# Kernel tuning notes

Measured on AMD Instinct MI355X. Metric: run time of the kernel, lower is better.

## Reference

```python
import jax, jax.numpy as jnp
import numpy as np

B, A, V, D = 16, 1024, 1024, 512


def setup_inputs() -> dict:
    key = jax.random.key(0)
    k1, k2 = jax.random.split(key)
    audio_encoded = jax.random.normal(k1, (B, A, D), dtype=jnp.float32)
    visual_encoded = jax.random.normal(k2, (B, V, D), dtype=jnp.float32)
    return {"audio_encoded": audio_encoded, "visual_encoded": visual_encoded}


def reference(audio_encoded, visual_encoded):
    # Batched pairwise L2 distance: out[b, a, v] = ||audio[b,a] - visual[b,v]||_2
    # Fused ||a||^2 + ||v||^2 - 2 a.v formulation (single batched GEMM) replacing
    # the original per-(batch, audio-frame) Python loop of diff/pow/sum/sqrt.
    a_sq = jnp.sum(audio_encoded * audio_encoded, axis=-1)   # [B, A]
    v_sq = jnp.sum(visual_encoded * visual_encoded, axis=-1)  # [B, V]
    cross = jnp.einsum("bad,bvd->bav", audio_encoded, visual_encoded)  # [B, A, V]
    dist_sq = a_sq[:, :, None] + v_sq[:, None, :] - 2.0 * cross
    dist_sq = jnp.maximum(dist_sq, 0.0)  # clamp fp round-off negatives
    l2_features = jnp.sqrt(dist_sq)  # [B, A, V]
    return l2_features
```

## Files before the change

### kernel.cpp

```cpp
#include <hip/hip_runtime.h>
#include <hip/hip_bf16.h>
#include <stdint.h>

typedef __attribute__((ext_vector_type(8))) short short8;
typedef __attribute__((ext_vector_type(4))) float fv4;
typedef __attribute__((ext_vector_type(4))) int   iv4;

constexpr int B_ = 16, A_ = 1024, V_ = 1024, D_ = 512;
constexpr int ROWS_A = B_ * A_;
constexpr int ROWS_T = 2 * ROWS_A;
constexpr size_t BF_BYTES_ONE = (size_t)ROWS_A * D_ * 2;
constexpr size_t WS_NEED = 2 * BF_BYTES_ONE + (size_t)ROWS_T * 4;

__device__ __forceinline__ unsigned f2bf(float f) {
    unsigned u = __builtin_bit_cast(unsigned, f);
    return (u + 0x7fffu + ((u >> 16) & 1u)) >> 16;
}

__global__ void __launch_bounds__(256)
convert_kernel(const float* __restrict__ audio, const float* __restrict__ visual,
               ushort* __restrict__ abf, ushort* __restrict__ vbf,
               float* __restrict__ normA, float* __restrict__ normV)
{
    const int lane = threadIdx.x & 63;
    const int wv   = (blockIdx.x * 256 + threadIdx.x) >> 6;
    const int nw   = (gridDim.x * 256) >> 6;

    for (int row = wv; row < ROWS_T; row += nw) {
        const float* src; ushort* dst; float* nd; int r;
        if (row < ROWS_A) { src = audio;  dst = abf; nd = normA; r = row; }
        else              { src = visual; dst = vbf; nd = normV; r = row - ROWS_A; }

        const float* p = src + (size_t)r * D_ + lane * 8;
        fv4 x0 = *(const fv4*)p;
        fv4 x1 = *(const fv4*)(p + 4);

        float s = 0.f;
#pragma unroll
        for (int i = 0; i < 4; ++i) s += x0[i] * x0[i] + x1[i] * x1[i];

        iv4 w;
        w[0] = (int)(f2bf(x0[0]) | (f2bf(x0[1]) << 16));
        w[1] = (int)(f2bf(x0[2]) | (f2bf(x0[3]) << 16));
        w[2] = (int)(f2bf(x1[0]) | (f2bf(x1[1]) << 16));
        w[3] = (int)(f2bf(x1[2]) | (f2bf(x1[3]) << 16));
        *(iv4*)(dst + (size_t)r * D_ + lane * 8) = w;

#pragma unroll
        for (int m = 1; m < 64; m <<= 1) s += __shfl_xor(s, m, 64);
        if (lane == 0) nd[r] = s;
    }
}

__device__ __forceinline__ void gload16(const void* g, void* l) {
    __builtin_amdgcn_global_load_lds((const __attribute__((address_space(1))) void*)g,
                                     (__attribute__((address_space(3))) void*)l,
                                     16, 0, 0);
}

__global__ void __launch_bounds__(256, 4)
gemm_kernel(const ushort* __restrict__ abf, const ushort* __restrict__ vbf,
            const float* __restrict__ normA, const float* __restrict__ normV,
            float* __restrict__ out)
{
    __shared__ __align__(16) char sA[128 * 128];
    __shared__ __align__(16) char sV[128 * 128];
    __shared__ float lnrm[256];

    const int t    = threadIdx.x;
    const int lane = t & 63;
    const int w    = t >> 6;
    const int wm   = w >> 1;
    const int wn   = w & 1;

    const int orig = blockIdx.x;
    const int wg   = (orig & 7) * 128 + (orig >> 3);
    const int b    = wg >> 6;
    const int tt   = wg & 63;
    const int ab   = tt >> 3;
    const int vb   = tt & 7;

    const ushort* Ag = abf + ((size_t)b * A_ + (size_t)ab * 128) * D_;
    const ushort* Vg = vbf + ((size_t)b * V_ + (size_t)vb * 128) * D_;

    const int rl = lane >> 3;
    const int cs = (lane & 7) ^ rl;

    fv4 acc[4][4];
#pragma unroll
    for (int i = 0; i < 4; ++i)
#pragma unroll
        for (int j = 0; j < 4; ++j) acc[i][j] = fv4{0.f, 0.f, 0.f, 0.f};

    const int frow = lane & 15;
    const int fg   = lane >> 4;
    const int xk   = frow & 7;

    for (int kt = 0; kt < D_ / 64; ++kt) {
#pragma unroll
        for (int i = 0; i < 4; ++i) {
            const int row = i * 32 + w * 8 + rl;
            gload16(Ag + (size_t)row * D_ + kt * 64 + cs * 8, sA + (i * 32 + w * 8) * 128);
            gload16(Vg + (size_t)row * D_ + kt * 64 + cs * 8, sV + (i * 32 + w * 8) * 128);
        }
        __syncthreads();

#pragma unroll
        for (int kk = 0; kk < 2; ++kk) {
            short8 af[4], vf[4];
#pragma unroll
            for (int m = 0; m < 4; ++m) {
                const int r = wm * 64 + m * 16 + frow;
                af[m] = *(const short8*)(sA + r * 128 + (((kk * 4 + fg) ^ xk) << 4));
            }
#pragma unroll
            for (int n = 0; n < 4; ++n) {
                const int r = wn * 64 + n * 16 + frow;
                vf[n] = *(const short8*)(sV + r * 128 + (((kk * 4 + fg) ^ xk) << 4));
            }
#pragma unroll
            for (int m = 0; m < 4; ++m)
#pragma unroll
                for (int n = 0; n < 4; ++n)
                    acc[m][n] = __builtin_amdgcn_mfma_f32_16x16x32_bf16(
                        af[m], vf[n], acc[m][n], 0, 0, 0);
        }
        __syncthreads();
    }

    if (t < 128) lnrm[t]       = normA[(size_t)b * A_ + ab * 128 + t];
    else         lnrm[t]       = normV[(size_t)b * V_ + vb * 128 + (t - 128)];
    __syncthreads();

    float* Ob = out + (size_t)b * A_ * V_ + ((size_t)ab * 128) * V_ + vb * 128;
#pragma unroll
    for (int m = 0; m < 4; ++m) {
#pragma unroll
        for (int n = 0; n < 4; ++n) {
            const int col = wn * 64 + n * 16 + frow;
            const float vsq = lnrm[128 + col];
#pragma unroll
            for (int j = 0; j < 4; ++j) {
                const int row = wm * 64 + m * 16 + fg * 4 + j;
                float d2 = lnrm[row] + vsq - 2.f * acc[m][n][j];
                Ob[(size_t)row * V_ + col] = sqrtf(fmaxf(d2, 0.f));
            }
        }
    }
}

__device__ __forceinline__ iv4 pack8(fv4 x, fv4 y) {
    iv4 r;
    r[0] = (int)(f2bf(x[0]) | (f2bf(x[1]) << 16));
    r[1] = (int)(f2bf(x[2]) | (f2bf(x[3]) << 16));
    r[2] = (int)(f2bf(y[0]) | (f2bf(y[1]) << 16));
    r[3] = (int)(f2bf(y[2]) | (f2bf(y[3]) << 16));
    return r;
}
__device__ __forceinline__ int slot_addr(int r, int g) {
    return r * 64 + (((g) ^ ((r >> 1) & 3)) << 4);
}

__global__ void __launch_bounds__(256)
l2dist_fused(const float* __restrict__ audio, const float* __restrict__ visual,
             float* __restrict__ out)
{
    __shared__ __align__(16) char sA[128 * 64];
    __shared__ __align__(16) char sV[128 * 64];
    __shared__ float pA[128][4];
    __shared__ float pV[128][4];
    __shared__ float nA[128];
    __shared__ float nV[128];

    const int t = threadIdx.x, lane = t & 63, wave = t >> 6;
    const int wm = wave >> 1, wn = wave & 1;
    const int vb = blockIdx.x, ab = blockIdx.y, b = blockIdx.z;
    const int r0 = t >> 2, g = t & 3;

    const float* Ap = audio  + ((size_t)b * A_ + (size_t)ab * 128) * D_;
    const float* Vp = visual + ((size_t)b * V_ + (size_t)vb * 128) * D_;

    fv4 acc[4][4];
#pragma unroll
    for (int i = 0; i < 4; ++i)
#pragma unroll
        for (int j = 0; j < 4; ++j) acc[i][j] = fv4{0.f, 0.f, 0.f, 0.f};
    float psA0 = 0.f, psA1 = 0.f, psV0 = 0.f, psV1 = 0.f;
    const int frow = lane & 15, fg = lane >> 4;

    for (int kt = 0; kt < 16; ++kt) {
        const int koff = kt * 32 + g * 8;
        fv4 a0 = *(const fv4*)(Ap + (size_t)r0 * D_ + koff);
        fv4 a1 = *(const fv4*)(Ap + (size_t)r0 * D_ + koff + 4);
        fv4 a2 = *(const fv4*)(Ap + (size_t)(r0 + 64) * D_ + koff);
        fv4 a3 = *(const fv4*)(Ap + (size_t)(r0 + 64) * D_ + koff + 4);
        fv4 v0 = *(const fv4*)(Vp + (size_t)r0 * D_ + koff);
        fv4 v1 = *(const fv4*)(Vp + (size_t)r0 * D_ + koff + 4);
        fv4 v2 = *(const fv4*)(Vp + (size_t)(r0 + 64) * D_ + koff);
        fv4 v3 = *(const fv4*)(Vp + (size_t)(r0 + 64) * D_ + koff + 4);
#pragma unroll
        for (int i = 0; i < 4; ++i) {
            psA0 += a0[i] * a0[i] + a1[i] * a1[i];
            psA1 += a2[i] * a2[i] + a3[i] * a3[i];
            psV0 += v0[i] * v0[i] + v1[i] * v1[i];
            psV1 += v2[i] * v2[i] + v3[i] * v3[i];
        }
        iv4 wa0 = pack8(a0, a1), wa1 = pack8(a2, a3);
        iv4 wv0 = pack8(v0, v1), wv1 = pack8(v2, v3);
        __syncthreads();
        *(iv4*)(sA + slot_addr(r0, g)) = wa0;
        *(iv4*)(sA + slot_addr(r0 + 64, g)) = wa1;
        *(iv4*)(sV + slot_addr(r0, g)) = wv0;
        *(iv4*)(sV + slot_addr(r0 + 64, g)) = wv1;
        __syncthreads();
        short8 af[4], bfr[4];
#pragma unroll
        for (int m = 0; m < 4; ++m)
            af[m] = *(const short8*)(sA + slot_addr(wm * 64 + m * 16 + frow, fg));
#pragma unroll
        for (int n = 0; n < 4; ++n)
            bfr[n] = *(const short8*)(sV + slot_addr(wn * 64 + n * 16 + frow, fg));
#pragma unroll
        for (int m = 0; m < 4; ++m)
#pragma unroll
            for (int n = 0; n < 4; ++n)
                acc[m][n] = __builtin_amdgcn_mfma_f32_16x16x32_bf16(af[m], bfr[n], acc[m][n], 0, 0, 0);
    }

    pA[r0][g] = psA0; pA[r0 + 64][g] = psA1;
    pV[r0][g] = psV0; pV[r0 + 64][g] = psV1;
    __syncthreads();
    if (t < 128) nA[t] = pA[t][0] + pA[t][1] + pA[t][2] + pA[t][3];
    else { int r = t - 128; nV[r] = pV[r][0] + pV[r][1] + pV[r][2] + pV[r][3]; }
    __syncthreads();

    float* Ob = out + (size_t)b * A_ * V_ + ((size_t)ab * 128) * V_ + vb * 128;
#pragma unroll
    for (int m = 0; m < 4; ++m)
#pragma unroll
        for (int n = 0; n < 4; ++n) {
            const int col = wn * 64 + n * 16 + frow;
            const float vsq = nV[col];
#pragma unroll
            for (int j = 0; j < 4; ++j) {
                const int row = wm * 64 + m * 16 + fg * 4 + j;
                float d2 = nA[row] + vsq - 2.f * acc[m][n][j];
                Ob[(size_t)row * V_ + col] = sqrtf(fmaxf(d2, 0.f));
            }
        }
}

extern "C" void kernel_launch(void* const* d_in, const int* in_sizes, int n_in,
                              void* d_out, int out_size, void* d_ws, size_t ws_size,
                              hipStream_t stream) {
    const float* audio  = (const float*)d_in[0];
    const float* visual = (const float*)d_in[1];
    float* out = (float*)d_out;

    if (ws_size >= WS_NEED) {
        char* ws = (char*)d_ws;
        ushort* abf = (ushort*)ws;
        ushort* vbf = (ushort*)(ws + BF_BYTES_ONE);
        float*  nA  = (float*)(ws + 2 * BF_BYTES_ONE);
        float*  nV  = nA + ROWS_A;
        convert_kernel<<<2048, 256, 0, stream>>>(audio, visual, abf, vbf, nA, nV);
        gemm_kernel<<<1024, 256, 0, stream>>>(abf, vbf, nA, nV, out);
    } else {
        dim3 grid(8, 8, 16);
        l2dist_fused<<<grid, 256, 0, stream>>>(audio, visual, out);
    }
}
```

Baseline: 46.33 us.

## Replace 128x128 GEMM with double-buffered 256x256 tile kernel using 512 threads

Swaps the 128x128 bf16 MFMA GEMM for a 256x256-tile kernel with 8 waves. It double-buffers LDS so the next K-slice's global-to-LDS loads overlap the current compute, uses inline ds_read_b128 with staged fragment loads and s_setprio around MFMA bursts, and preloads the norms before the main loop. The aim is more data reuse per tile and hidden load latency. The cost is 128KB of LDS per block and only 256 workgroups, which is about one per CU, so occupancy and tail balance may suffer.

Result: slower. 49.54 us (+6.9%).

```diff
diff --git a/kernel.cpp b/kernel.cpp
--- a/kernel.cpp
+++ b/kernel.cpp
@@ -9,8 +9,8 @@
 constexpr int B_ = 16, A_ = 1024, V_ = 1024, D_ = 512;
 constexpr int ROWS_A = B_ * A_;
 constexpr int ROWS_T = 2 * ROWS_A;
-constexpr size_t BF_BYTES_ONE = (size_t)ROWS_A * D_ * 2;
-constexpr size_t WS_NEED = 2 * BF_BYTES_ONE + (size_t)ROWS_T * 4;
+constexpr size_t BF_ONE = (size_t)ROWS_A * D_ * 2;
+constexpr size_t WS_NEED = 2 * BF_ONE + (size_t)ROWS_T * 4;
 
 __device__ __forceinline__ unsigned f2bf(float f) {
     unsigned u = __builtin_bit_cast(unsigned, f);
@@ -57,91 +57,164 @@
                                      (__attribute__((address_space(3))) void*)l,
                                      16, 0, 0);
 }
-
-__global__ void __launch_bounds__(256, 4)
-gemm_kernel(const ushort* __restrict__ abf, const ushort* __restrict__ vbf,
-            const float* __restrict__ normA, const float* __restrict__ normV,
-            float* __restrict__ out)
+__device__ __forceinline__ unsigned lds_addr(const void* p) {
+    return (unsigned)(unsigned long long)(__attribute__((address_space(3))) const char*)p;
+}
+__device__ __forceinline__ short8 dsr128(unsigned a) {
+    short8 r;
+    asm volatile("ds_read_b128 %0, %1" : "=v"(r) : "v"(a));
+    return r;
+}
+#define LGK0() asm volatile("s_waitcnt lgkmcnt(0)")
+#define VMC0() asm volatile("s_waitcnt vmcnt(0)")
+#define SB0()  __builtin_amdgcn_sched_barrier(0)
+#define BAR()  __builtin_amdgcn_s_barrier()
+
+__global__ void __launch_bounds__(512, 2)
+gemm256(const ushort* __restrict__ abf, const ushort* __restrict__ vbf,
+        const float* __restrict__ normA, const float* __restrict__ normV,
+        float* __restrict__ out)
 {
-    __shared__ __align__(16) char sA[128 * 128];
-    __shared__ __align__(16) char sV[128 * 128];
-    __shared__ float lnrm[256];
-
-    const int t    = threadIdx.x;
-    const int lane = t & 63;
-    const int w    = t >> 6;
-    const int wm   = w >> 1;
-    const int wn   = w & 1;
+    __shared__ __align__(16) char sA[2][256 * 128];
+    __shared__ __align__(16) char sB[2][256 * 128];
+    __shared__ float lnrm[512];
+
+    const int t = threadIdx.x, lane = t & 63, w = t >> 6;
+    const int wm = w >> 2, wn = w & 3;
 
     const int orig = blockIdx.x;
-    const int wg   = (orig & 7) * 128 + (orig >> 3);
-    const int b    = wg >> 6;
-    const int tt   = wg & 63;
-    const int ab   = tt >> 3;
-    const int vb   = tt & 7;
-
-    const ushort* Ag = abf + ((size_t)b * A_ + (size_t)ab * 128) * D_;
-    const ushort* Vg = vbf + ((size_t)b * V_ + (size_t)vb * 128) * D_;
+    const int wg   = (orig & 7) * 32 + (orig >> 3);
+    const int b = wg >> 4, tile = wg & 15, ab = tile >> 2, vb = tile & 3;
+
+    const ushort* Ag = abf + ((size_t)b * A_ + ab * 256) * D_;
+    const ushort* Vg = vbf + ((size_t)b * V_ + vb * 256) * D_;
 
     const int rl = lane >> 3;
     const int cs = (lane & 7) ^ rl;
-
-    fv4 acc[4][4];
-#pragma unroll
-    for (int i = 0; i < 4; ++i)
-#pragma unroll
-        for (int j = 0; j < 4; ++j) acc[i][j] = fv4{0.f, 0.f, 0.f, 0.f};
-
-    const int frow = lane & 15;
-    const int fg   = lane >> 4;
-    const int xk   = frow & 7;
-
-    for (int kt = 0; kt < D_ / 64; ++kt) {
-#pragma unroll
-        for (int i = 0; i < 4; ++i) {
-            const int row = i * 32 + w * 8 + rl;
-            gload16(Ag + (size_t)row * D_ + kt * 64 + cs * 8, sA + (i * 32 + w * 8) * 128);
-            gload16(Vg + (size_t)row * D_ + kt * 64 + cs * 8, sV + (i * 32 + w * 8) * 128);
-        }
-        __syncthreads();
-
-#pragma unroll
-        for (int kk = 0; kk < 2; ++kk) {
-            short8 af[4], vf[4];
-#pragma unroll
-            for (int m = 0; m < 4; ++m) {
-                const int r = wm * 64 + m * 16 + frow;
-                af[m] = *(const short8*)(sA + r * 128 + (((kk * 4 + fg) ^ xk) << 4));
+    const ushort* asrc = Ag + (size_t)(w * 8 + rl) * D_ + cs * 8;
+    const ushort* vsrc = Vg + (size_t)(w * 8 + rl) * D_ + cs * 8;
+
+    if (t < 256) lnrm[t] = normA[(size_t)b * A_ + ab * 256 + t];
+    else         lnrm[t] = normV[(size_t)b * V_ + vb * 256 + (t - 256)];
+    __syncthreads();
+
+    fv4 acc[8][4];
+#pragma unroll
+    for (int m = 0; m < 8; ++m)
+#pragma unroll
+        for (int n = 0; n < 4; ++n) acc[m][n] = fv4{0.f, 0.f, 0.f, 0.f};
+
+    const int frow = lane & 15, fg = lane >> 4, xk = frow & 7;
+    const unsigned sAbase = lds_addr(&sA[0][0]);
+    const unsigned sBbase = lds_addr(&sB[0][0]);
+    const unsigned arow = (unsigned)((wm * 128 + frow) * 128);
+    const unsigned brow = (unsigned)((wn * 64 + frow) * 128);
+    const unsigned c0 = (unsigned)(((0 + fg) ^ xk) << 4);
+    const unsigned c1 = (unsigned)(((4 + fg) ^ xk) << 4);
+
+#pragma unroll
+    for (int h = 0; h < 4; ++h) {
+        gload16(asrc + (size_t)h * 64 * D_, (char*)sA[0] + (h * 64 + w * 8) * 128);
+        gload16(vsrc + (size_t)h * 64 * D_, (char*)sB[0] + (h * 64 + w * 8) * 128);
+    }
+    VMC0();
+
+    short8 av[4][2], bv[4][2];
+
+    for (int kt = 0; kt < 8; ++kt) {
+        BAR();
+        const int cur = kt & 1;
+
+        if (kt < 7) {
+            const size_t soff = (size_t)(kt + 1) * 64;
+            char* da = (char*)sA[cur ^ 1] + w * 8 * 128;
+            char* db = (char*)sB[cur ^ 1] + w * 8 * 128;
+#pragma unroll
+            for (int h = 0; h < 4; ++h) {
+                gload16(asrc + (size_t)h * 64 * D_ + soff, da + h * 64 * 128);
+                gload16(vsrc + (size_t)h * 64 * D_ + soff, db + h * 64 * 128);
             }
-#pragma unroll
-            for (int n = 0; n < 4; ++n) {
-                const int r = wn * 64 + n * 16 + frow;
-                vf[n] = *(const short8*)(sV + r * 128 + (((kk * 4 + fg) ^ xk) << 4));
-            }
+        }
+
+        const unsigned Ab = sAbase + (unsigned)cur * 32768u + arow;
+        const unsigned Bb = sBbase + (unsigned)cur * 32768u + brow;
+
+#pragma unroll
+        for (int m = 0; m < 4; ++m) {
+            av[m][0] = dsr128(Ab + m * 2048 + c0);
+            av[m][1] = dsr128(Ab + m * 2048 + c1);
+        }
+#pragma unroll
+        for (int n = 0; n < 2; ++n) {
+            bv[n][0] = dsr128(Bb + n * 2048 + c0);
+            bv[n][1] = dsr128(Bb + n * 2048 + c1);
+        }
+        LGK0(); SB0();
+        __builtin_amdgcn_s_setprio(1);
+#pragma unroll
+        for (int k = 0; k < 2; ++k)
 #pragma unroll
             for (int m = 0; m < 4; ++m)
 #pragma unroll
-                for (int n = 0; n < 4; ++n)
-                    acc[m][n] = __builtin_amdgcn_mfma_f32_16x16x32_bf16(
-                        af[m], vf[n], acc[m][n], 0, 0, 0);
-        }
-        __syncthreads();
-    }
-
-    if (t < 128) lnrm[t]       = normA[(size_t)b * A_ + ab * 128 + t];
-    else         lnrm[t]       = normV[(size_t)b * V_ + vb * 128 + (t - 128)];
-    __syncthreads();
-
-    float* Ob = out + (size_t)b * A_ * V_ + ((size_t)ab * 128) * V_ + vb * 128;
-#pragma unroll
-    for (int m = 0; m < 4; ++m) {
+                for (int n = 0; n < 2; ++n)
+                    acc[m][n] = __builtin_amdgcn_mfma_f32_16x16x32_bf16(av[m][k], bv[n][k], acc[m][n], 0, 0, 0);
+        __builtin_amdgcn_s_setprio(0);
+
+#pragma unroll
+        for (int n = 2; n < 4; ++n) {
+            bv[n][0] = dsr128(Bb + n * 2048 + c0);
+            bv[n][1] = dsr128(Bb + n * 2048 + c1);
+        }
+        LGK0(); SB0();
+        __builtin_amdgcn_s_setprio(1);
+#pragma unroll
+        for (int k = 0; k < 2; ++k)
+#pragma unroll
+            for (int m = 0; m < 4; ++m)
+#pragma unroll
+                for (int n = 2; n < 4; ++n)
+                    acc[m][n] = __builtin_amdgcn_mfma_f32_16x16x32_bf16(av[m][k], bv[n][k], acc[m][n], 0, 0, 0);
+        __builtin_amdgcn_s_setprio(0);
+
+#pragma unroll
+        for (int m = 0; m < 4; ++m) {
+            av[m][0] = dsr128(Ab + (m + 4) * 2048 + c0);
+            av[m][1] = dsr128(Ab + (m + 4) * 2048 + c1);
+        }
+        LGK0(); SB0();
+        __builtin_amdgcn_s_setprio(1);
+#pragma unroll
+        for (int k = 0; k < 2; ++k)
+#pragma unroll
+            for (int m = 0; m < 4; ++m)
+#pragma unroll
+                for (int n = 2; n < 4; ++n)
+                    acc[m + 4][n] = __builtin_amdgcn_mfma_f32_16x16x32_bf16(av[m][k], bv[n][k], acc[m + 4][n], 0, 0, 0);
+        __builtin_amdgcn_s_setprio(0);
+
+        __builtin_amdgcn_s_setprio(1);
+#pragma unroll
+        for (int k = 0; k < 2; ++k)
+#pragma unroll
+            for (int m = 0; m < 4; ++m)
+#pragma unroll
+                for (int n = 0; n < 2; ++n)
+                    acc[m + 4][n] = __builtin_amdgcn_mfma_f32_16x16x32_bf16(av[m][k], bv[n][k], acc[m + 4][n], 0, 0, 0);
+        __builtin_amdgcn_s_setprio(0);
+
+        VMC0();
+    }
+
+    float* Ob = out + (size_t)b * A_ * V_ + (size_t)(ab * 256) * V_ + vb * 256;
+#pragma unroll
+    for (int m = 0; m < 8; ++m) {
 #pragma unroll
         for (int n = 0; n < 4; ++n) {
             const int col = wn * 64 + n * 16 + frow;
-            const float vsq = lnrm[128 + col];
+            const float vsq = lnrm[256 + col];
 #pragma unroll
             for (int j = 0; j < 4; ++j) {
-                const int row = wm * 64 + m * 16 + fg * 4 + j;
+                const int row = wm * 128 + m * 16 + fg * 4 + j;
                 float d2 = lnrm[row] + vsq - 2.f * acc[m][n][j];
                 Ob[(size_t)row * V_ + col] = sqrtf(fmaxf(d2, 0.f));
             }
@@ -165,8 +238,8 @@
 l2dist_fused(const float* __restrict__ audio, const float* __restrict__ visual,
              float* __restrict__ out)
 {
-    __shared__ __align__(16) char sA[128 * 64];
-    __shared__ __align__(16) char sV[128 * 64];
+    __shared__ __align__(16) char lA[128 * 64];
+    __shared__ __align__(16) char lV[128 * 64];
     __shared__ float pA[128][4];
     __shared__ float pV[128][4];
     __shared__ float nA[128];
@@ -208,18 +281,18 @@
         iv4 wa0 = pack8(a0, a1), wa1 = pack8(a2, a3);
         iv4 wv0 = pack8(v0, v1), wv1 = pack8(v2, v3);
         __syncthreads();
-        *(iv4*)(sA + slot_addr(r0, g)) = wa0;
-        *(iv4*)(sA + slot_addr(r0 + 64, g)) = wa1;
-        *(iv4*)(sV + slot_addr(r0, g)) = wv0;
-        *(iv4*)(sV + slot_addr(r0 + 64, g)) = wv1;
+        *(iv4*)(lA + slot_addr(r0, g)) = wa0;
+        *(iv4*)(lA + slot_addr(r0 + 64, g)) = wa1;
+        *(iv4*)(lV + slot_addr(r0, g)) = wv0;
+        *(iv4*)(lV + slot_addr(r0 + 64, g)) = wv1;
         __syncthreads();
         short8 af[4], bfr[4];
 #pragma unroll
         for (int m = 0; m < 4; ++m)
-            af[m] = *(const short8*)(sA + slot_addr(wm * 64 + m * 16 + frow, fg));
+            af[m] = *(const short8*)(lA + slot_addr(wm * 64 + m * 16 + frow, fg));
 #pragma unroll
         for (int n = 0; n < 4; ++n)
-            bfr[n] = *(const short8*)(sV + slot_addr(wn * 64 + n * 16 + frow, fg));
+            bfr[n] = *(const short8*)(lV + slot_addr(wn * 64 + n * 16 + frow, fg));
 #pragma unroll
         for (int m = 0; m < 4; ++m)
 #pragma unroll
@@ -260,11 +333,11 @@
     if (ws_size >= WS_NEED) {
         char* ws = (char*)d_ws;
         ushort* abf = (ushort*)ws;
-        ushort* vbf = (ushort*)(ws + BF_BYTES_ONE);
-        float*  nA  = (float*)(ws + 2 * BF_BYTES_ONE);
+        ushort* vbf = (ushort*)(ws + BF_ONE);
+        float*  nA  = (float*)(ws + 2 * BF_ONE);
         float*  nV  = nA + ROWS_A;
         convert_kernel<<<2048, 256, 0, stream>>>(audio, visual, abf, vbf, nA, nV);
-        gemm_kernel<<<1024, 256, 0, stream>>>(abf, vbf, nA, nV, out);
+        gemm256<<<256, 512, 0, stream>>>(abf, vbf, nA, nV, out);
     } else {
         dim3 grid(8, 8, 16);
         l2dist_fused<<<grid, 256, 0, stream>>>(audio, visual, out);
```
